# Performance work log

Hardware: AMD Instinct MI355X
Metric: run time of the kernel (lower is better)

The kernel has to match this reference:

```python
import jax, jax.numpy as jnp
import numpy as np
from math import sqrt

D_MODEL = 768
D_T = 256
N_HEADS = 12
HEAD_DIM = D_MODEL // N_HEADS
SCALE = sqrt(HEAD_DIM)


def setup_inputs() -> dict:
    key = jax.random.key(0)
    ks = jax.random.split(key, 11)
    b, l = 8, 1024
    inv = 1.0 / sqrt(D_MODEL)
    inv_t = 1.0 / sqrt(D_T)
    return {
        "x": jax.random.normal(ks[0], (b, l, D_MODEL), dtype=jnp.float32),
        "t": jax.random.normal(ks[1], (b, D_T), dtype=jnp.float32),
        "rel_pos_bias": jax.random.normal(ks[2], (N_HEADS, l, l), dtype=jnp.float32),
        # torch Linear weights: [out_features, in_features]
        "Wx_q": jax.random.normal(ks[3], (D_MODEL, D_MODEL), dtype=jnp.float32) * inv,
        "Wx_k": jax.random.normal(ks[4], (D_MODEL, D_MODEL), dtype=jnp.float32) * inv,
        "Wx_v": jax.random.normal(ks[5], (D_MODEL, D_MODEL), dtype=jnp.float32) * inv,
        "Wt_q": jax.random.normal(ks[6], (D_MODEL, D_T), dtype=jnp.float32) * inv_t,
        "Wt_k": jax.random.normal(ks[7], (D_MODEL, D_T), dtype=jnp.float32) * inv_t,
        "Wt_v": jax.random.normal(ks[8], (D_MODEL, D_T), dtype=jnp.float32) * inv_t,
        "W_o": jax.random.normal(ks[9], (D_MODEL, D_MODEL), dtype=jnp.float32) * inv,
        "b_o": jax.random.normal(ks[10], (D_MODEL,), dtype=jnp.float32) * 0.01,
    }


def _split_heads(y):
    # [b, l, n*d] -> [b, n, l, d]
    b, l, _ = y.shape
    return y.reshape(b, l, N_HEADS, HEAD_DIM).transpose(0, 2, 1, 3)


def reference(x, t, rel_pos_bias, Wx_q, Wx_k, Wx_v, Wt_q, Wt_k, Wt_v, W_o, b_o):
    # time-conditioned QKV: per-batch additive shift broadcast over seq
    q = _split_heads(x @ Wx_q.T + (t @ Wt_q.T)[:, None, :])
    k = _split_heads(x @ Wx_k.T + (t @ Wt_k.T)[:, None, :])
    v = _split_heads(x @ Wx_v.T + (t @ Wt_v.T)[:, None, :])
    attn = jnp.einsum("bnld,bnmd->bnlm", q, k) / SCALE
    attn = attn + rel_pos_bias  # [n,l,l] broadcasts over batch
    probs = jax.nn.softmax(attn, axis=-1)
    o = jnp.einsum("bnlm,bnmd->bnld", probs, v)
    b, _, l, _ = o.shape
    o = o.transpose(0, 2, 1, 3).reshape(b, l, D_MODEL)
    return o @ W_o.T + b_o
```

## Files before the change

kernel.cpp:

```cpp
#include <hip/hip_runtime.h>
#include <hip/hip_bf16.h>
#include <stdint.h>

typedef __bf16 bf16_t;
typedef __attribute__((ext_vector_type(8))) __bf16 bf16x8;
typedef __attribute__((ext_vector_type(4))) __bf16 bf16x4;
typedef __attribute__((ext_vector_type(4))) float f32x4;

#define DEVI __device__ __forceinline__

DEVI void gll16(const void* g, void* lds_base_wave_uniform) {
  __builtin_amdgcn_global_load_lds(
      (const __attribute__((address_space(1))) uint32_t*)(uintptr_t)g,
      (__attribute__((address_space(3))) uint32_t*)(uintptr_t)lds_base_wave_uniform,
      16, 0, 0);
}

__global__ void cvt_f32_to_bf16(const float* __restrict__ src, bf16_t* __restrict__ dst, int n) {
  int i = (blockIdx.x * blockDim.x + threadIdx.x) * 4;
  if (i >= n) return;
  float4 v = *(const float4*)(src + i);
  bf16x4 o = {(bf16_t)v.x, (bf16_t)v.y, (bf16_t)v.z, (bf16_t)v.w};
  *(bf16x4*)(dst + i) = o;
}

__global__ void cvt_scale_bf16(const float* __restrict__ src, bf16_t* __restrict__ dst, int n) {
  int i = (blockIdx.x * blockDim.x + threadIdx.x) * 4;
  if (i >= n) return;
  const float s = 1.44269504088896f;
  float4 v = *(const float4*)(src + i);
  bf16x4 o = {(bf16_t)(v.x * s), (bf16_t)(v.y * s), (bf16_t)(v.z * s), (bf16_t)(v.w * s)};
  *(bf16x4*)(dst + i) = o;
}

__global__ void shift_kernel(const float* __restrict__ t,
                             const float* __restrict__ wtq,
                             const float* __restrict__ wtk,
                             const float* __restrict__ wtv,
                             float* __restrict__ shift) {
  int idx = blockIdx.x * blockDim.x + threadIdx.x;
  if (idx >= 8 * 2304) return;
  int b = idx / 2304, n = idx % 2304;
  const float* w = (n < 768) ? (wtq + (size_t)n * 256)
                 : (n < 1536) ? (wtk + (size_t)(n - 768) * 256)
                              : (wtv + (size_t)(n - 1536) * 256);
  const float4* tv = (const float4*)(t + (size_t)b * 256);
  const float4* wv = (const float4*)w;
  float acc = 0.f;
#pragma unroll 8
  for (int i = 0; i < 64; i++) {
    float4 a = tv[i], c = wv[i];
    acc += a.x * c.x + a.y * c.y + a.z * c.z + a.w * c.w;
  }
  shift[idx] = acc;
}

template <int MODE>
__global__ __launch_bounds__(256, 2) void gemm_bt(
    const bf16_t* __restrict__ A, const bf16_t* __restrict__ B,
    const float* __restrict__ add, void* __restrict__ Cout,
    int M, int N, int K) {
  __shared__ alignas(16) bf16_t As[128 * 32];
  __shared__ alignas(16) bf16_t Bs[128 * 32];
  const int t = threadIdx.x, l = t & 63, w = t >> 6;
  const int wr = w >> 1, wc = w & 1;
  const int bm = blockIdx.x, bn = blockIdx.y;

  f32x4 acc[4][4] = {};

  const int srow = t >> 2;
  const int scol = (t & 3) * 8;
  const bf16_t* Ab = A + ((size_t)bm * 128 + srow) * K + scol;
  const bf16_t* Bb = B + ((size_t)bn * 128 + srow) * K + scol;
  char* AsB = (char*)As + w * 1024;
  char* BsB = (char*)Bs + w * 1024;
  const size_t K64 = (size_t)64 * K;

  const int ro = (l & 15) * 32 + (l >> 4) * 8;
  const bf16_t* ApA = As + (wr * 64) * 32 + ro;
  const bf16_t* BpB = Bs + (wc * 64) * 32 + ro;

  for (int k0 = 0; k0 < K; k0 += 32) {
    __syncthreads();
    gll16(Ab + k0, AsB);
    gll16(Ab + K64 + k0, AsB + 4096);
    gll16(Bb + k0, BsB);
    gll16(Bb + K64 + k0, BsB + 4096);
    __syncthreads();
    bf16x8 af[4], bfr[4];
#pragma unroll
    for (int i = 0; i < 4; i++) {
      af[i]  = *(const bf16x8*)(ApA + i * 16 * 32);
      bfr[i] = *(const bf16x8*)(BpB + i * 16 * 32);
    }
#pragma unroll
    for (int mi = 0; mi < 4; mi++)
#pragma unroll
      for (int ni = 0; ni < 4; ni++)
        acc[mi][ni] = __builtin_amdgcn_mfma_f32_16x16x32_bf16(af[mi], bfr[ni], acc[mi][ni], 0, 0, 0);
  }

  const int row0 = bm * 128 + wr * 64 + (l >> 4) * 4;
  const int col0 = bn * 128 + wc * 64 + (l & 15);
  if (MODE == 0) {
    bf16_t* C = (bf16_t*)Cout;
    const float* sh = add + (size_t)((bm * 128) >> 10) * N;
#pragma unroll
    for (int ni = 0; ni < 4; ni++) {
      const int col = col0 + ni * 16;
      const float s0 = sh[col];
#pragma unroll
      for (int mi = 0; mi < 4; mi++)
#pragma unroll
        for (int i = 0; i < 4; i++)
          C[(size_t)(row0 + mi * 16 + i) * N + col] = (bf16_t)(acc[mi][ni][i] + s0);
    }
  } else {
    float* C = (float*)Cout;
#pragma unroll
    for (int ni = 0; ni < 4; ni++) {
      const int col = col0 + ni * 16;
      const float s0 = add[col];
#pragma unroll
      for (int mi = 0; mi < 4; mi++)
#pragma unroll
        for (int i = 0; i < 4; i++)
          C[(size_t)(row0 + mi * 16 + i) * N + col] = acc[mi][ni][i] + s0;
    }
  }
}

__global__ __launch_bounds__(256, 2) void attn_fused(
    const bf16_t* __restrict__ qkv,
    const bf16_t* __restrict__ biasb,
    bf16_t* __restrict__ o) {
  const int id = blockIdx.x;
  const int slot = id >> 3;
  const int qt = slot & 15;
  const int grp = (id & 7) + 8 * (slot >> 4);
  const int h = grp % 12, b = grp / 12;
  const int t = threadIdx.x, l = t & 63, w = t >> 6;
  const int sl = l & 15, g = l >> 4;

  __shared__ alignas(16) bf16_t Ks[2][64 * 64];
  __shared__ alignas(16) bf16_t Bi[2][64 * 64];
  __shared__ alignas(16) bf16_t Vt[2][64 * 64];
  __shared__ alignas(16) bf16_t Ps[4][16 * 64];

  const size_t rowb = (size_t)b * 1024;
  const int qrow = qt * 64 + w * 16 + sl;

  bf16x8 qf[2];
  {
    const bf16_t* qp = qkv + (rowb + qrow) * 2304 + h * 64 + g * 8;
    qf[0] = *(const bf16x8*)qp;
    qf[1] = *(const bf16x8*)(qp + 32);
  }
  __builtin_amdgcn_sched_barrier(0);

  const int st_row = w * 16 + (l >> 3);
  const int st_chk = (l & 7) ^ (l >> 3);
  const bf16_t* ksrc = qkv + rowb * 2304 + 768 + h * 64;
  const bf16_t* bsrc = biasb + ((size_t)h << 20) + (size_t)(qt * 64) * 1024;

  auto STAGE = [&](int buf, int kt2) {
    const bf16_t* k0 = ksrc + (size_t)(kt2 * 64 + st_row) * 2304 + st_chk * 8;
    gll16(k0,            (char*)Ks[buf] + w * 2048);
    gll16(k0 + 8 * 2304, (char*)Ks[buf] + w * 2048 + 1024);
    const bf16_t* b0 = bsrc + (size_t)st_row * 1024 + kt2 * 64 + st_chk * 8;
    gll16(b0,            (char*)Bi[buf] + w * 2048);
    gll16(b0 + 8 * 1024, (char*)Bi[buf] + w * 2048 + 1024);
  };
  auto VLOAD = [&](int kt2, bf16x8& a, bf16x8& bq) {
    const bf16_t* vp = qkv + (rowb + kt2 * 64 + l) * 2304 + 1536 + h * 64 + w * 16;
    a = *(const bf16x8*)vp;
    bq = *(const bf16x8*)(vp + 8);
  };
  auto VSCAT = [&](int buf, const bf16x8& a, const bf16x8& bq) {
#pragma unroll
    for (int j = 0; j < 16; j++) {
      const int d = w * 16 + j;
      const int addr = d * 64 + (((l >> 3) ^ (d & 7)) * 8) + (l & 7);
      Vt[buf][addr] = (j < 8) ? a[j] : bq[j - 8];
    }
  };

  float m_run = -INFINITY, l_run = 0.f;
  f32x4 oacc[4] = {};
  const float C1 = 0.125f * 1.44269504088896f;

  bf16x8 va0, va1, vb0, vb1;

  VLOAD(0, va0, va1);
  __builtin_amdgcn_sched_barrier(0);
  STAGE(0, 0);
  __builtin_amdgcn_sched_barrier(0);
  VLOAD(1, vb0, vb1);
  __builtin_amdgcn_sched_barrier(0);
  VSCAT(0, va0, va1);
  asm volatile("s_waitcnt vmcnt(2) lgkmcnt(0)" ::: "memory");
  __builtin_amdgcn_s_barrier();
  __builtin_amdgcn_sched_barrier(0);

#pragma unroll 2
  for (int kt = 0; kt < 16; kt++) {
    const int cur = kt & 1, nxt = cur ^ 1;

    if (kt + 1 < 16) {
      STAGE(nxt, kt + 1);
      __builtin_amdgcn_sched_barrier(0);
    }
    if (kt + 2 < 16) {
      if (cur == 0) VLOAD(kt + 2, va0, va1);
      else          VLOAD(kt + 2, vb0, vb1);
      __builtin_amdgcn_sched_barrier(0);
    }
    if (kt + 1 < 16) {
      if (cur == 0) VSCAT(nxt, vb0, vb1);
      else          VSCAT(nxt, va0, va1);
    }

    f32x4 sv[4];
    __builtin_amdgcn_s_setprio(1);
#pragma unroll
    for (int nf = 0; nf < 4; nf++) {
      const char* base = (const char*)Ks[cur] + (16 * nf + sl) * 128;
      bf16x8 kf0 = *(const bf16x8*)(base + ((g ^ (sl & 7)) * 16));
      bf16x8 kf1 = *(const bf16x8*)(base + (((4 + g) ^ (sl & 7)) * 16));
      f32x4 z = {0.f, 0.f, 0.f, 0.f};
      z = __builtin_amdgcn_mfma_f32_16x16x32_bf16(kf0, qf[0], z, 0, 0, 0);
      z = __builtin_amdgcn_mfma_f32_16x16x32_bf16(kf1, qf[1], z, 0, 0, 0);
      sv[nf] = z;
    }
    __builtin_amdgcn_s_setprio(0);

    float lg[4][4];
    {
      const char* bb = (const char*)Bi[cur] + (w * 16 + sl) * 128 + (g & 1) * 8;
#pragma unroll
      for (int nf = 0; nf < 4; nf++) {
        bf16x4 bq = *(const bf16x4*)(bb + (((2 * nf + (g >> 1)) ^ (sl & 7)) * 16));
#pragma unroll
        for (int i = 0; i < 4; i++)
          lg[nf][i] = fmaf(sv[nf][i], C1, (float)bq[i]);
      }
    }

    float mx = fmaxf(fmaxf(fmaxf(lg[0][0], lg[0][1]), fmaxf(lg[0][2], lg[0][3])),
                     fmaxf(fmaxf(lg[1][0], lg[1][1]), fmaxf(lg[1][2], lg[1][3])));
    mx = fmaxf(mx, fmaxf(fmaxf(fmaxf(lg[2][0], lg[2][1]), fmaxf(lg[2][2], lg[2][3])),
                         fmaxf(fmaxf(lg[3][0], lg[3][1]), fmaxf(lg[3][2], lg[3][3]))));
    mx = fmaxf(mx, __shfl_xor(mx, 16));
    mx = fmaxf(mx, __shfl_xor(mx, 32));

    if (!__all(mx - m_run <= 8.0f)) {
      const float mnew = fmaxf(m_run, mx);
      const float alpha = exp2f(m_run - mnew);
      m_run = mnew;
      l_run *= alpha;
#pragma unroll
      for (int i = 0; i < 4; i++) {
        const float a_pv = __shfl(alpha, g * 4 + i);
#pragma unroll
        for (int nf2 = 0; nf2 < 4; nf2++) oacc[nf2][i] *= a_pv;
      }
    }

    float rs = 0.f;
#pragma unroll
    for (int nf = 0; nf < 4; nf++)
#pragma unroll
      for (int i = 0; i < 4; i++) {
        lg[nf][i] = exp2f(lg[nf][i] - m_run);
        rs += lg[nf][i];
      }
    rs += __shfl_xor(rs, 16);
    rs += __shfl_xor(rs, 32);
    l_run += rs;

    bf16_t* Pw = Ps[w];
    {
      char* pb = (char*)Pw + sl * 128 + (g & 1) * 8;
#pragma unroll
      for (int nf = 0; nf < 4; nf++) {
        bf16x4 pk = {(bf16_t)lg[nf][0], (bf16_t)lg[nf][1], (bf16_t)lg[nf][2], (bf16_t)lg[nf][3]};
        *(bf16x4*)(pb + ((2 * nf + (g >> 1)) ^ (sl & 7)) * 16) = pk;
      }
    }
    bf16x8 pf[2];
#pragma unroll
    for (int c = 0; c < 2; c++)
      pf[c] = *(const bf16x8*)((char*)Pw + sl * 128 + ((4 * c + g) ^ (sl & 7)) * 16);

    __builtin_amdgcn_s_setprio(1);
#pragma unroll
    for (int nf2 = 0; nf2 < 4; nf2++) {
      const int d = nf2 * 16 + sl;
      const bf16_t* vb = Vt[cur] + d * 64;
      bf16x8 vf0 = *(const bf16x8*)(vb + ((g ^ (d & 7)) * 8));
      bf16x8 vf1 = *(const bf16x8*)(vb + (((g + 4) ^ (d & 7)) * 8));
      oacc[nf2] = __builtin_amdgcn_mfma_f32_16x16x32_bf16(pf[0], vf0, oacc[nf2], 0, 0, 0);
      oacc[nf2] = __builtin_amdgcn_mfma_f32_16x16x32_bf16(pf[1], vf1, oacc[nf2], 0, 0, 0);
    }
    __builtin_amdgcn_s_setprio(0);

    if (kt + 1 < 16) {
      if (kt + 2 < 16) asm volatile("s_waitcnt vmcnt(2) lgkmcnt(0)" ::: "memory");
      else             asm volatile("s_waitcnt vmcnt(0) lgkmcnt(0)" ::: "memory");
      __builtin_amdgcn_s_barrier();
      __builtin_amdgcn_sched_barrier(0);
    }
  }

#pragma unroll
  for (int i = 0; i < 4; i++) {
    const float inv = 1.0f / __shfl(l_run, g * 4 + i);
    const size_t row = rowb + qt * 64 + w * 16 + g * 4 + i;
#pragma unroll
    for (int nf2 = 0; nf2 < 4; nf2++)
      o[row * 768 + h * 64 + nf2 * 16 + sl] = (bf16_t)(oacc[nf2][i] * inv);
  }
}

extern "C" void kernel_launch(void* const* d_in, const int* in_sizes, int n_in,
                              void* d_out, int out_size, void* d_ws, size_t ws_size,
                              hipStream_t stream) {
  const float* x    = (const float*)d_in[0];
  const float* tin  = (const float*)d_in[1];
  const float* bias = (const float*)d_in[2];
  const float* Wxq  = (const float*)d_in[3];
  const float* Wxk  = (const float*)d_in[4];
  const float* Wxv  = (const float*)d_in[5];
  const float* Wtq  = (const float*)d_in[6];
  const float* Wtk  = (const float*)d_in[7];
  const float* Wtv  = (const float*)d_in[8];
  const float* Wo   = (const float*)d_in[9];
  const float* bo   = (const float*)d_in[10];
  float* out = (float*)d_out;

  char* ws = (char*)d_ws;
  bf16_t* x_bf    = (bf16_t*)(ws);
  bf16_t* wcat    = (bf16_t*)(ws + 12582912);
  bf16_t* wo_bf   = (bf16_t*)(ws + 16121856);
  float*  shift   = (float*) (ws + 17301504);
  bf16_t* qkvb    = (bf16_t*)(ws + 17375232);
  bf16_t* obuf    = (bf16_t*)(ws + 55123968);
  bf16_t* bias_bf = (bf16_t*)(ws + 67706880);

  const int W = 768 * 768;
  cvt_f32_to_bf16<<<6144, 256, 0, stream>>>(x, x_bf, 8192 * 768);
  cvt_f32_to_bf16<<<576, 256, 0, stream>>>(Wxq, wcat, W);
  cvt_f32_to_bf16<<<576, 256, 0, stream>>>(Wxk, wcat + W, W);
  cvt_f32_to_bf16<<<576, 256, 0, stream>>>(Wxv, wcat + 2 * W, W);
  cvt_f32_to_bf16<<<576, 256, 0, stream>>>(Wo, wo_bf, W);
  cvt_scale_bf16<<<12288, 256, 0, stream>>>(bias, bias_bf, 12 * 1024 * 1024);
  shift_kernel<<<72, 256, 0, stream>>>(tin, Wtq, Wtk, Wtv, shift);
  gemm_bt<0><<<dim3(64, 18), 256, 0, stream>>>(x_bf, wcat, shift, qkvb, 8192, 2304, 768);
  attn_fused<<<1536, 256, 0, stream>>>(qkvb, bias_bf, obuf);
  gemm_bt<1><<<dim3(64, 6), 256, 0, stream>>>(obuf, wo_bf, bo, out, 8192, 768, 768);
}
```

Measured before the change: 316.3 us.

## Double-buffer GEMM LDS tiles and load attention bias straight into registers

The GEMM main loop gets two LDS buffers, so the next K-tile's async global-to-LDS loads are issued before the current tile's MFMAs, with one barrier per step instead of two. In the attention kernel, the relative-position bias no longer goes through an LDS tile: each lane loads its own bf16x4 bias fragments directly into registers, one iteration ahead, and the waitcnt values are adjusted to match. Dropping the bias LDS buffer shrinks shared memory, and launch bounds rise to 4 blocks per CU for higher occupancy. The trade-offs are less coalesced per-lane bias reads from global memory and more register pressure under the tighter launch bound.

```diff
diff --git a/kernel.cpp b/kernel.cpp
--- a/kernel.cpp
+++ b/kernel.cpp
@@ -60,8 +60,8 @@
     const bf16_t* __restrict__ A, const bf16_t* __restrict__ B,
     const float* __restrict__ add, void* __restrict__ Cout,
     int M, int N, int K) {
-  __shared__ alignas(16) bf16_t As[128 * 32];
-  __shared__ alignas(16) bf16_t Bs[128 * 32];
+  __shared__ alignas(16) bf16_t As[2][128 * 32];
+  __shared__ alignas(16) bf16_t Bs[2][128 * 32];
   const int t = threadIdx.x, l = t & 63, w = t >> 6;
   const int wr = w >> 1, wc = w & 1;
   const int bm = blockIdx.x, bn = blockIdx.y;
@@ -72,32 +72,49 @@
   const int scol = (t & 3) * 8;
   const bf16_t* Ab = A + ((size_t)bm * 128 + srow) * K + scol;
   const bf16_t* Bb = B + ((size_t)bn * 128 + srow) * K + scol;
-  char* AsB = (char*)As + w * 1024;
-  char* BsB = (char*)Bs + w * 1024;
   const size_t K64 = (size_t)64 * K;
 
-  const int ro = (l & 15) * 32 + (l >> 4) * 8;
-  const bf16_t* ApA = As + (wr * 64) * 32 + ro;
-  const bf16_t* BpB = Bs + (wc * 64) * 32 + ro;
-
-  for (int k0 = 0; k0 < K; k0 += 32) {
-    __syncthreads();
+  auto STAGE = [&](int buf, int k0) {
+    char* AsB = (char*)As[buf] + w * 1024;
+    char* BsB = (char*)Bs[buf] + w * 1024;
     gll16(Ab + k0, AsB);
     gll16(Ab + K64 + k0, AsB + 4096);
     gll16(Bb + k0, BsB);
     gll16(Bb + K64 + k0, BsB + 4096);
-    __syncthreads();
+  };
+
+  const int ro = (l & 15) * 32 + (l >> 4) * 8;
+  const int NT = K / 32;
+
+  STAGE(0, 0);
+  asm volatile("s_waitcnt vmcnt(0)" ::: "memory");
+  __builtin_amdgcn_s_barrier();
+  __builtin_amdgcn_sched_barrier(0);
+
+  for (int tt = 0; tt < NT; tt++) {
+    const int cur = tt & 1;
+    if (tt + 1 < NT) {
+      STAGE(cur ^ 1, (tt + 1) * 32);
+      __builtin_amdgcn_sched_barrier(0);
+    }
+    const bf16_t* Ap = As[cur] + (wr * 64) * 32 + ro;
+    const bf16_t* Bp = Bs[cur] + (wc * 64) * 32 + ro;
     bf16x8 af[4], bfr[4];
 #pragma unroll
     for (int i = 0; i < 4; i++) {
-      af[i]  = *(const bf16x8*)(ApA + i * 16 * 32);
-      bfr[i] = *(const bf16x8*)(BpB + i * 16 * 32);
+      af[i]  = *(const bf16x8*)(Ap + i * 16 * 32);
+      bfr[i] = *(const bf16x8*)(Bp + i * 16 * 32);
     }
 #pragma unroll
     for (int mi = 0; mi < 4; mi++)
 #pragma unroll
       for (int ni = 0; ni < 4; ni++)
         acc[mi][ni] = __builtin_amdgcn_mfma_f32_16x16x32_bf16(af[mi], bfr[ni], acc[mi][ni], 0, 0, 0);
+    if (tt + 1 < NT) {
+      asm volatile("s_waitcnt vmcnt(0) lgkmcnt(0)" ::: "memory");
+      __builtin_amdgcn_s_barrier();
+      __builtin_amdgcn_sched_barrier(0);
+    }
   }
 
   const int row0 = bm * 128 + wr * 64 + (l >> 4) * 4;
@@ -130,7 +147,7 @@
   }
 }
 
-__global__ __launch_bounds__(256, 2) void attn_fused(
+__global__ __launch_bounds__(256, 4) void attn_fused(
     const bf16_t* __restrict__ qkv,
     const bf16_t* __restrict__ biasb,
     bf16_t* __restrict__ o) {
@@ -143,7 +160,6 @@
   const int sl = l & 15, g = l >> 4;
 
   __shared__ alignas(16) bf16_t Ks[2][64 * 64];
-  __shared__ alignas(16) bf16_t Bi[2][64 * 64];
   __shared__ alignas(16) bf16_t Vt[2][64 * 64];
   __shared__ alignas(16) bf16_t Ps[4][16 * 64];
 
@@ -161,15 +177,12 @@
   const int st_row = w * 16 + (l >> 3);
   const int st_chk = (l & 7) ^ (l >> 3);
   const bf16_t* ksrc = qkv + rowb * 2304 + 768 + h * 64;
-  const bf16_t* bsrc = biasb + ((size_t)h << 20) + (size_t)(qt * 64) * 1024;
-
-  auto STAGE = [&](int buf, int kt2) {
+  const bf16_t* bsrc = biasb + ((size_t)h << 20) + (size_t)qrow * 1024 + g * 4;
+
+  auto STAGEK = [&](int buf, int kt2) {
     const bf16_t* k0 = ksrc + (size_t)(kt2 * 64 + st_row) * 2304 + st_chk * 8;
     gll16(k0,            (char*)Ks[buf] + w * 2048);
     gll16(k0 + 8 * 2304, (char*)Ks[buf] + w * 2048 + 1024);
-    const bf16_t* b0 = bsrc + (size_t)st_row * 1024 + kt2 * 64 + st_chk * 8;
-    gll16(b0,            (char*)Bi[buf] + w * 2048);
-    gll16(b0 + 8 * 1024, (char*)Bi[buf] + w * 2048 + 1024);
   };
   auto VLOAD = [&](int kt2, bf16x8& a, bf16x8& bq) {
     const bf16_t* vp = qkv + (rowb + kt2 * 64 + l) * 2304 + 1536 + h * 64 + w * 16;
@@ -190,15 +203,22 @@
   const float C1 = 0.125f * 1.44269504088896f;
 
   bf16x8 va0, va1, vb0, vb1;
+  bf16x4 biasA[4], biasB[4];
 
   VLOAD(0, va0, va1);
   __builtin_amdgcn_sched_barrier(0);
-  STAGE(0, 0);
+  STAGEK(0, 0);
+  __builtin_amdgcn_sched_barrier(0);
+  {
+    const bf16_t* bb = bsrc;
+#pragma unroll
+    for (int nf = 0; nf < 4; nf++) biasA[nf] = *(const bf16x4*)(bb + nf * 16);
+  }
   __builtin_amdgcn_sched_barrier(0);
   VLOAD(1, vb0, vb1);
   __builtin_amdgcn_sched_barrier(0);
   VSCAT(0, va0, va1);
-  asm volatile("s_waitcnt vmcnt(2) lgkmcnt(0)" ::: "memory");
+  asm volatile("s_waitcnt vmcnt(6) lgkmcnt(0)" ::: "memory");
   __builtin_amdgcn_s_barrier();
   __builtin_amdgcn_sched_barrier(0);
 
@@ -207,7 +227,11 @@
     const int cur = kt & 1, nxt = cur ^ 1;
 
     if (kt + 1 < 16) {
-      STAGE(nxt, kt + 1);
+      STAGEK(nxt, kt + 1);
+      __builtin_amdgcn_sched_barrier(0);
+      const bf16_t* bb = bsrc + (kt + 1) * 64;
+#pragma unroll
+      for (int nf = 0; nf < 4; nf++) biasB[nf] = *(const bf16x4*)(bb + nf * 16);
       __builtin_amdgcn_sched_barrier(0);
     }
     if (kt + 2 < 16) {
@@ -235,16 +259,11 @@
     __builtin_amdgcn_s_setprio(0);
 
     float lg[4][4];
-    {
-      const char* bb = (const char*)Bi[cur] + (w * 16 + sl) * 128 + (g & 1) * 8;
-#pragma unroll
-      for (int nf = 0; nf < 4; nf++) {
-        bf16x4 bq = *(const bf16x4*)(bb + (((2 * nf + (g >> 1)) ^ (sl & 7)) * 16));
-#pragma unroll
-        for (int i = 0; i < 4; i++)
-          lg[nf][i] = fmaf(sv[nf][i], C1, (float)bq[i]);
-      }
-    }
+#pragma unroll
+    for (int nf = 0; nf < 4; nf++)
+#pragma unroll
+      for (int i = 0; i < 4; i++)
+        lg[nf][i] = fmaf(sv[nf][i], C1, (float)biasA[nf][i]);
 
     float mx = fmaxf(fmaxf(fmaxf(lg[0][0], lg[0][1]), fmaxf(lg[0][2], lg[0][3])),
                      fmaxf(fmaxf(lg[1][0], lg[1][1]), fmaxf(lg[1][2], lg[1][3])));
@@ -305,8 +324,9 @@
     __builtin_amdgcn_s_setprio(0);
 
     if (kt + 1 < 16) {
-      if (kt + 2 < 16) asm volatile("s_waitcnt vmcnt(2) lgkmcnt(0)" ::: "memory");
-      else             asm volatile("s_waitcnt vmcnt(0) lgkmcnt(0)" ::: "memory");
+#pragma unroll
+      for (int nf = 0; nf < 4; nf++) biasA[nf] = biasB[nf];
+      asm volatile("s_waitcnt vmcnt(2) lgkmcnt(0)" ::: "memory");
       __builtin_amdgcn_s_barrier();
       __builtin_amdgcn_sched_barrier(0);
     }
```

Measured after the change: 303.1 us. 1.04x faster.
